# Performance work log

Hardware: AMD Instinct MI355X
Metric: run time of the kernel (lower is better)

Reference implementation:

```python
import jax, jax.numpy as jnp
import numpy as np

N_USERS = 100000
N_ITEMS = 50000
D = 64
NNZ = 4_800_000
N_HOPS = 3


def setup_inputs() -> dict:
    key = jax.random.key(0)
    k1, k2, k3, k4, k5 = jax.random.split(key, 5)
    n_nodes = N_USERS + N_ITEMS
    user_embed = jax.random.normal(k1, (N_USERS, D), dtype=jnp.float32) * 0.1
    item_embed = jax.random.normal(k2, (N_ITEMS, D), dtype=jnp.float32) * 0.1
    # COO indices of the symmetric-normalized interaction adjacency
    row = jax.random.randint(k3, (NNZ,), 0, n_nodes, dtype=jnp.int32)
    col = jax.random.randint(k4, (NNZ,), 0, n_nodes, dtype=jnp.int32)
    # normalized adjacency values ~ 1/deg scale
    vals = jax.random.uniform(k5, (NNZ,), dtype=jnp.float32) * (1.0 / 32.0)
    return {"user_embed": user_embed, "item_embed": item_embed,
            "row": row, "col": col, "vals": vals}


def reference(user_embed, item_embed, row, col, vals):
    """GraphConv.forward with perturbed=False (path used in M4.forward).

    torch.sparse.mm(A, X) over COO == segment_sum(vals * X[col], row).
    """
    n_users = user_embed.shape[0]
    n_nodes = n_users + item_embed.shape[0]
    ego = jnp.concatenate([user_embed, item_embed], axis=0)  # [N, D]

    def spmm(x):
        return jax.ops.segment_sum(vals[:, None] * x[col], row,
                                   num_segments=n_nodes)

    hop_outs = []
    for _ in range(N_HOPS):
        ego = spmm(ego)
        hop_outs.append(ego)
    layer_embeddings = hop_outs[0]  # k == 0 hop (layer_cl path)
    all_embeddings = jnp.mean(jnp.stack(hop_outs, axis=1), axis=1)  # [N, D]

    return (all_embeddings[:n_users], all_embeddings[n_users:],
            layer_embeddings[:n_users], layer_embeddings[n_users:])
```

## Files before the change

### kernel.cpp

```cpp
#include <hip/hip_runtime.h>
#include <hip/hip_bf16.h>


#define D 64
typedef unsigned short u16;

#define NBP   512
#define BSH   9
#define TILE  2048
#define FCAP  4608

__device__ __forceinline__ float bf2f(u16 h) {
    union { unsigned int u; float f; } c;
    c.u = ((unsigned int)h) << 16;
    return c.f;
}
__device__ __forceinline__ u16 f2bf(float f) {
    union { float f; unsigned int u; } c; c.f = f;
    unsigned int r = c.u + 0x7FFFu + ((c.u >> 16) & 1u);
    return (u16)(r >> 16);
}

struct U4 { u16 a, b, c, d; } __attribute__((aligned(8)));

__global__ void detect_kernel(const u16* __restrict__ emb,
                              const u16* __restrict__ vals,
                              int* __restrict__ flags) {
    int lane = threadIdx.x;
    int se = 0, sv = 0;
    for (int k = 0; k < 16; ++k) {
        int idx = (lane * 16 + k) * 2;
        u16 he = emb[idx];
        int ee = (he >> 7) & 0xFF;
        if (ee >= 100 && ee < 127) se++;
        u16 hv = vals[idx];
        int ev = (hv >> 7) & 0xFF;
        if ((hv >> 15) == 0 && ev >= 60 && ev < 123) sv++;
    }
    atomicAdd(&flags[0], se);
    atomicAdd(&flags[1], sv);
}

__global__ __launch_bounds__(256)
void convert_kernel(const void* __restrict__ ue, const void* __restrict__ ie,
                    const int* __restrict__ flags, u16* __restrict__ x0,
                    int total, int usz) {
    int i = (blockIdx.x * blockDim.x + threadIdx.x) * 4;
    if (i >= total) return;
    const void* src = (i < usz) ? ue : ie;
    int off = (i < usz) ? i : i - usz;
    U4 o;
    if (flags[0] >= 512) {
        o = *(const U4*)((const u16*)src + off);
    } else {
        const float4 v = *(const float4*)((const float*)src + off);
        o.a = f2bf(v.x); o.b = f2bf(v.y); o.c = f2bf(v.z); o.d = f2bf(v.w);
    }
    *(U4*)(x0 + i) = o;
}

__global__ __launch_bounds__(256)
void bhist_kernel(const int* __restrict__ row, int* __restrict__ bcnt, int nnz) {
    __shared__ int h[NBP];
    int t = threadIdx.x;
    h[t] = 0; h[t + 256] = 0;
    __syncthreads();
    for (int i = blockIdx.x * 256 + t; i < nnz; i += gridDim.x * 256)
        atomicAdd(&h[row[i] >> BSH], 1);
    __syncthreads();
    if (h[t])       atomicAdd(&bcnt[t],       h[t]);
    if (h[t + 256]) atomicAdd(&bcnt[t + 256], h[t + 256]);
}

__global__ void bscan_kernel(const int* __restrict__ bcnt, int* __restrict__ bbase,
                             int* __restrict__ bcursor, int nb, int nnz) {
    __shared__ int buf[NBP];
    int t = threadIdx.x;
    int v = (t < nb) ? bcnt[t] : 0;
    buf[t] = v;
    __syncthreads();
    for (int off = 1; off < NBP; off <<= 1) {
        int y = (t >= off) ? buf[t - off] : 0;
        __syncthreads();
        buf[t] += y;
        __syncthreads();
    }
    int excl = buf[t] - v;
    bbase[t] = excl;
    bcursor[t] = excl;
    if (t == 0) bbase[nb] = nnz;
}

__global__ __launch_bounds__(256)
void coarse_kernel(const int* __restrict__ row, const int* __restrict__ col,
                   const void* __restrict__ vals, const int* __restrict__ flags,
                   int* __restrict__ bcursor, int2* __restrict__ es2, int nnz) {
    __shared__ int2 ebuf[TILE];
    __shared__ u16  slotb[TILE];
    __shared__ int  hcnt[NBP], hscn[NBP], goff[NBP];
    int t = threadIdx.x;
    int base = blockIdx.x * TILE;
    int tcnt = nnz - base; if (tcnt > TILE) tcnt = TILE;
    bool vbf = (flags[1] >= 512);

    hcnt[t] = 0; hcnt[t + 256] = 0;
    __syncthreads();

    int eb[8], er[8], ep[8], ev[8];
#pragma unroll
    for (int k = 0; k < 8; ++k) {
        int i = base + k * 256 + t;
        eb[k] = -1;
        if (k * 256 + t < tcnt) {
            int r = row[i];
            int c = col[i];
            float v = vbf ? bf2f(((const u16*)vals)[i]) : ((const float*)vals)[i];
            eb[k] = r >> BSH;
            ep[k] = ((r & 511) << 18) | c;
            ev[k] = __float_as_int(v);
            er[k] = atomicAdd(&hcnt[eb[k]], 1);
        }
    }
    __syncthreads();
    hscn[t] = hcnt[t]; hscn[t + 256] = hcnt[t + 256];
    __syncthreads();
    for (int off = 1; off < NBP; off <<= 1) {
        int a0 = (t >= off) ? hscn[t - off] : 0;
        int a1 = (t + 256 >= off) ? hscn[t + 256 - off] : 0;
        __syncthreads();
        hscn[t] += a0; hscn[t + 256] += a1;
        __syncthreads();
    }
#pragma unroll
    for (int k = 0; k < 8; ++k) {
        if (eb[k] >= 0) {
            int slot = hscn[eb[k]] - hcnt[eb[k]] + er[k];
            ebuf[slot] = make_int2(ep[k], ev[k]);
            slotb[slot] = (u16)eb[k];
        }
    }
    __syncthreads();
    if (hcnt[t] > 0)       goff[t]       = atomicAdd(&bcursor[t],       hcnt[t]);
    if (hcnt[t + 256] > 0) goff[t + 256] = atomicAdd(&bcursor[t + 256], hcnt[t + 256]);
    __syncthreads();
#pragma unroll
    for (int k = 0; k < 8; ++k) {
        int p = k * 256 + t;
        if (p < tcnt) {
            int b = slotb[p];
            int dest = goff[b] + (p - (hscn[b] - hcnt[b]));
            es2[dest] = ebuf[p];
        }
    }
}

__global__ __launch_bounds__(512)
void fine_kernel(const int2* __restrict__ es2, const int* __restrict__ bbase,
                 int2* __restrict__ es, int* __restrict__ rp, int n, int nnz) {
    __shared__ int2 obuf[FCAP];
    __shared__ int hist[512], scn[512], cur[128];
    int b = blockIdx.x, t = threadIdx.x;
    int r0 = b << BSH;
    int s = bbase[b], e = bbase[b + 1];
    if (b == 0 && t == 0) rp[n] = nnz;

    hist[t] = 0;
    __syncthreads();
    for (int i = s + t; i < e; i += 512)
        atomicAdd(&hist[(unsigned)es2[i].x >> 18], 1);
    __syncthreads();
    scn[t] = hist[t];
    __syncthreads();
    for (int off = 1; off < 512; off <<= 1) {
        int a = (t >= off) ? scn[t - off] : 0;
        __syncthreads();
        scn[t] += a;
        __syncthreads();
    }
    {
        int ex = scn[t] - hist[t];
        int r = r0 + t;
        if (r < n) rp[r] = s + ex;
    }

    for (int c = 0; c < 4; ++c) {
        int qb = c * 128;
        int q0 = qb ? scn[qb - 1] : 0;
        int qcnt = scn[qb + 127] - q0;
        int ds = s + q0;
        bool fit = (qcnt <= FCAP);
        if (t < 128) {
            int ex = scn[qb + t] - hist[qb + t];
            cur[t] = fit ? (ex - q0) : (s + ex);
        }
        __syncthreads();
        if (fit) {
            for (int i = s + t; i < e; i += 512) {
                int2 p = es2[i];
                int rl = (unsigned)p.x >> 18;
                if ((rl >> 7) == c) {
                    int pos = atomicAdd(&cur[rl & 127], 1);
                    obuf[pos] = make_int2(p.x & 0x3FFFF, p.y);
                }
            }
            __syncthreads();
            for (int p2 = t; p2 < qcnt; p2 += 512)
                es[ds + p2] = obuf[p2];
            __syncthreads();
        } else {
            for (int i = s + t; i < e; i += 512) {
                int2 p = es2[i];
                int rl = (unsigned)p.x >> 18;
                if ((rl >> 7) == c) {
                    int pos = atomicAdd(&cur[rl & 127], 1);
                    es[pos] = make_int2(p.x & 0x3FFFF, p.y);
                }
            }
            __syncthreads();
        }
    }
}


__global__ __launch_bounds__(256)
void spmm_kernel(const u16* __restrict__ x, u16* __restrict__ y,
                 const int* __restrict__ rp, const int2* __restrict__ es, int n) {
    int wid  = (blockIdx.x * blockDim.x + threadIdx.x) >> 6;
    int lane = threadIdx.x & 63;
    int qt   = lane >> 4;
    int sub  = lane & 15;
    int r    = (wid << 2) + qt;
    int e = 0, e1 = 0;
    if (r < n) { e = rp[r]; e1 = rp[r + 1]; }
    const u16* xs = x + (sub << 2);

    float a0 = 0.f, a1 = 0.f, a2 = 0.f, a3 = 0.f;
    float b0 = 0.f, b1 = 0.f, b2 = 0.f, b3 = 0.f;

    for (; e + 8 <= e1; e += 8) {
        int2 p0 = es[e],     p1 = es[e + 1], p2 = es[e + 2], p3 = es[e + 3];
        int2 p4 = es[e + 4], p5 = es[e + 5], p6 = es[e + 6], p7 = es[e + 7];
        U4 v0 = *(const U4*)(xs + (p0.x << 6));
        U4 v1 = *(const U4*)(xs + (p1.x << 6));
        U4 v2 = *(const U4*)(xs + (p2.x << 6));
        U4 v3 = *(const U4*)(xs + (p3.x << 6));
        U4 v4 = *(const U4*)(xs + (p4.x << 6));
        U4 v5 = *(const U4*)(xs + (p5.x << 6));
        U4 v6 = *(const U4*)(xs + (p6.x << 6));
        U4 v7 = *(const U4*)(xs + (p7.x << 6));
        float w0 = __int_as_float(p0.y), w1 = __int_as_float(p1.y);
        float w2 = __int_as_float(p2.y), w3 = __int_as_float(p3.y);
        float w4 = __int_as_float(p4.y), w5 = __int_as_float(p5.y);
        float w6 = __int_as_float(p6.y), w7 = __int_as_float(p7.y);
        a0 += w0 * bf2f(v0.a); a1 += w0 * bf2f(v0.b); a2 += w0 * bf2f(v0.c); a3 += w0 * bf2f(v0.d);
        b0 += w1 * bf2f(v1.a); b1 += w1 * bf2f(v1.b); b2 += w1 * bf2f(v1.c); b3 += w1 * bf2f(v1.d);
        a0 += w2 * bf2f(v2.a); a1 += w2 * bf2f(v2.b); a2 += w2 * bf2f(v2.c); a3 += w2 * bf2f(v2.d);
        b0 += w3 * bf2f(v3.a); b1 += w3 * bf2f(v3.b); b2 += w3 * bf2f(v3.c); b3 += w3 * bf2f(v3.d);
        a0 += w4 * bf2f(v4.a); a1 += w4 * bf2f(v4.b); a2 += w4 * bf2f(v4.c); a3 += w4 * bf2f(v4.d);
        b0 += w5 * bf2f(v5.a); b1 += w5 * bf2f(v5.b); b2 += w5 * bf2f(v5.c); b3 += w5 * bf2f(v5.d);
        a0 += w6 * bf2f(v6.a); a1 += w6 * bf2f(v6.b); a2 += w6 * bf2f(v6.c); a3 += w6 * bf2f(v6.d);
        b0 += w7 * bf2f(v7.a); b1 += w7 * bf2f(v7.b); b2 += w7 * bf2f(v7.c); b3 += w7 * bf2f(v7.d);
    }
    for (; e < e1; ++e) {
        int2 p = es[e];
        U4 v = *(const U4*)(xs + (p.x << 6));
        float w = __int_as_float(p.y);
        a0 += w * bf2f(v.a); a1 += w * bf2f(v.b); a2 += w * bf2f(v.c); a3 += w * bf2f(v.d);
    }
    if (r < n) {
        U4 o;
        o.a = f2bf(a0 + b0); o.b = f2bf(a1 + b1);
        o.c = f2bf(a2 + b2); o.d = f2bf(a3 + b3);
        *(U4*)(y + (r << 6) + (sub << 2)) = o;
    }
}

__global__ __launch_bounds__(256)
void spmm_last_kernel(const u16* __restrict__ x2, const u16* __restrict__ x1,
                      float* __restrict__ out,
                      const int* __restrict__ rp, const int2* __restrict__ es, int n) {
    int wid  = (blockIdx.x * blockDim.x + threadIdx.x) >> 6;
    int lane = threadIdx.x & 63;
    int qt   = lane >> 4;
    int sub  = lane & 15;
    int r    = (wid << 2) + qt;
    int e = 0, e1 = 0;
    if (r < n) { e = rp[r]; e1 = rp[r + 1]; }
    const u16* xs = x2 + (sub << 2);

    float a0 = 0.f, a1 = 0.f, a2 = 0.f, a3 = 0.f;
    float b0 = 0.f, b1 = 0.f, b2 = 0.f, b3 = 0.f;

    for (; e + 8 <= e1; e += 8) {
        int2 p0 = es[e],     p1 = es[e + 1], p2 = es[e + 2], p3 = es[e + 3];
        int2 p4 = es[e + 4], p5 = es[e + 5], p6 = es[e + 6], p7 = es[e + 7];
        U4 v0 = *(const U4*)(xs + (p0.x << 6));
        U4 v1 = *(const U4*)(xs + (p1.x << 6));
        U4 v2 = *(const U4*)(xs + (p2.x << 6));
        U4 v3 = *(const U4*)(xs + (p3.x << 6));
        U4 v4 = *(const U4*)(xs + (p4.x << 6));
        U4 v5 = *(const U4*)(xs + (p5.x << 6));
        U4 v6 = *(const U4*)(xs + (p6.x << 6));
        U4 v7 = *(const U4*)(xs + (p7.x << 6));
        float w0 = __int_as_float(p0.y), w1 = __int_as_float(p1.y);
        float w2 = __int_as_float(p2.y), w3 = __int_as_float(p3.y);
        float w4 = __int_as_float(p4.y), w5 = __int_as_float(p5.y);
        float w6 = __int_as_float(p6.y), w7 = __int_as_float(p7.y);
        a0 += w0 * bf2f(v0.a); a1 += w0 * bf2f(v0.b); a2 += w0 * bf2f(v0.c); a3 += w0 * bf2f(v0.d);
        b0 += w1 * bf2f(v1.a); b1 += w1 * bf2f(v1.b); b2 += w1 * bf2f(v1.c); b3 += w1 * bf2f(v1.d);
        a0 += w2 * bf2f(v2.a); a1 += w2 * bf2f(v2.b); a2 += w2 * bf2f(v2.c); a3 += w2 * bf2f(v2.d);
        b0 += w3 * bf2f(v3.a); b1 += w3 * bf2f(v3.b); b2 += w3 * bf2f(v3.c); b3 += w3 * bf2f(v3.d);
        a0 += w4 * bf2f(v4.a); a1 += w4 * bf2f(v4.b); a2 += w4 * bf2f(v4.c); a3 += w4 * bf2f(v4.d);
        b0 += w5 * bf2f(v5.a); b1 += w5 * bf2f(v5.b); b2 += w5 * bf2f(v5.c); b3 += w5 * bf2f(v5.d);
        a0 += w6 * bf2f(v6.a); a1 += w6 * bf2f(v6.b); a2 += w6 * bf2f(v6.c); a3 += w6 * bf2f(v6.d);
        b0 += w7 * bf2f(v7.a); b1 += w7 * bf2f(v7.b); b2 += w7 * bf2f(v7.c); b3 += w7 * bf2f(v7.d);
    }
    for (; e < e1; ++e) {
        int2 p = es[e];
        U4 v = *(const U4*)(xs + (p.x << 6));
        float w = __int_as_float(p.y);
        a0 += w * bf2f(v.a); a1 += w * bf2f(v.b); a2 += w * bf2f(v.c); a3 += w * bf2f(v.d);
    }
    if (r < n) {
        int idx = (r << 6) + (sub << 2);
        U4 h1v = *(const U4*)(x1 + idx);
        U4 h2v = *(const U4*)(x2 + idx);
        float h1a = bf2f(h1v.a), h1b = bf2f(h1v.b), h1c = bf2f(h1v.c), h1d = bf2f(h1v.d);
        float h2a = bf2f(h2v.a), h2b = bf2f(h2v.b), h2c = bf2f(h2v.c), h2d = bf2f(h2v.d);
        float4 o;
        o.x = (h1a + h2a + (a0 + b0)) * (1.0f / 3.0f);
        o.y = (h1b + h2b + (a1 + b1)) * (1.0f / 3.0f);
        o.z = (h1c + h2c + (a2 + b2)) * (1.0f / 3.0f);
        o.w = (h1d + h2d + (a3 + b3)) * (1.0f / 3.0f);
        *(float4*)(out + idx) = o;
        float4 l;
        l.x = h1a; l.y = h1b; l.z = h1c; l.w = h1d;
        *(float4*)(out + (size_t)n * D + idx) = l;
    }
}


extern "C" void kernel_launch(void* const* d_in, const int* in_sizes, int n_in,
                              void* d_out, int out_size, void* d_ws, size_t ws_size,
                              hipStream_t stream) {
    const void* ue   = d_in[0];
    const void* ie   = d_in[1];
    const int*  row  = (const int*)d_in[2];
    const int*  col  = (const int*)d_in[3];
    const void* vals = d_in[4];

    const int nu  = in_sizes[0] / D;
    const int ni  = in_sizes[1] / D;
    const int n   = nu + ni;
    const int nnz = in_sizes[2];

    char* ws = (char*)d_ws;
    u16*  X0     = (u16*)ws;   ws += (size_t)n * D * sizeof(u16);
    u16*  X1     = (u16*)ws;   ws += (size_t)n * D * sizeof(u16);
    u16*  X2     = (u16*)ws;   ws += (size_t)n * D * sizeof(u16);
    int2* es2    = (int2*)X1;
    int2* es     = (int2*)ws;  ws += (size_t)nnz * sizeof(int2);
    int*  rp     = (int*)ws;   ws += (size_t)(n + 1) * sizeof(int);
    int*  bcnt   = (int*)ws;   ws += NBP * sizeof(int);
    int*  flags  = (int*)ws;   ws += 2 * sizeof(int);
    int*  bbase  = (int*)ws;   ws += (NBP + 1) * sizeof(int);
    int*  bcursor= (int*)ws;   ws += NBP * sizeof(int);

    const int tb = 256;
    const int rblocks = (n + 15) / 16;
    const int cblocks = (n * D / 4 + tb - 1) / tb;
    const int NB      = (n + 511) / 512;
    const int coarseb = (nnz + TILE - 1) / TILE;

    hipMemsetAsync(bcnt, 0, (NBP + 2) * sizeof(int), stream);
    detect_kernel <<<1, 64, 0, stream>>>((const u16*)ue, (const u16*)vals, flags);
    convert_kernel<<<cblocks, tb, 0, stream>>>(ue, ie, flags, X0, n * D, nu * D);
    bhist_kernel  <<<512, tb, 0, stream>>>(row, bcnt, nnz);
    bscan_kernel  <<<1, NBP, 0, stream>>>(bcnt, bbase, bcursor, NB, nnz);
    coarse_kernel <<<coarseb, tb, 0, stream>>>(row, col, vals, flags, bcursor, es2, nnz);
    fine_kernel   <<<NB, 512, 0, stream>>>(es2, bbase, es, rp, n, nnz);

    spmm_kernel     <<<rblocks, tb, 0, stream>>>(X0, X1, rp, es, n);
    spmm_kernel     <<<rblocks, tb, 0, stream>>>(X1, X2, rp, es, n);
    spmm_last_kernel<<<rblocks, tb, 0, stream>>>(X2, X1, (float*)d_out, rp, es, n);
}
```

Before: 610.3 us.

## Sub-sort edges within each row by column bucket in fine_kernel

In the in-shared-memory path of fine_kernel, edges are now bucketed by (row, column>>13) through an extra histogram pass and a block-wide scan, so each row's edges come out roughly ordered by column range. The goal is better locality for the gathers of x[col] in the SpMM hops. The cost is an extra pass over es2 per chunk, two more 4096-entry shared arrays that may lower occupancy, and more block-wide synchronisation in the preprocessing kernel.

New measurement: 660.6 us. +8.2%, slower.

```diff
diff --git a/kernel.cpp b/kernel.cpp
--- a/kernel.cpp
+++ b/kernel.cpp
@@ -9,6 +9,8 @@
 #define BSH   9
 #define TILE  2048
 #define FCAP  4608
+#define CGS   32
+#define KH    (128 * CGS)
 
 __device__ __forceinline__ float bf2f(u16 h) {
     union { unsigned int u; float f; } c;
@@ -158,7 +160,8 @@
 void fine_kernel(const int2* __restrict__ es2, const int* __restrict__ bbase,
                  int2* __restrict__ es, int* __restrict__ rp, int n, int nnz) {
     __shared__ int2 obuf[FCAP];
-    __shared__ int hist[512], scn[512], cur[128];
+    __shared__ int hist[512], scn[512], wsum[512], cur[128];
+    __shared__ int kh[KH], cur2[KH];
     int b = blockIdx.x, t = threadIdx.x;
     int r0 = b << BSH;
     int s = bbase[b], e = bbase[b + 1];
@@ -189,18 +192,47 @@
         int qcnt = scn[qb + 127] - q0;
         int ds = s + q0;
         bool fit = (qcnt <= FCAP);
-        if (t < 128) {
-            int ex = scn[qb + t] - hist[qb + t];
-            cur[t] = fit ? (ex - q0) : (s + ex);
-        }
-        __syncthreads();
         if (fit) {
+#pragma unroll
+            for (int j = 0; j < KH / 512; ++j) kh[t + j * 512] = 0;
+            __syncthreads();
             for (int i = s + t; i < e; i += 512) {
                 int2 p = es2[i];
                 int rl = (unsigned)p.x >> 18;
                 if ((rl >> 7) == c) {
-                    int pos = atomicAdd(&cur[rl & 127], 1);
-                    obuf[pos] = make_int2(p.x & 0x3FFFF, p.y);
+                    int key = ((rl & 127) << 5) | ((p.x & 0x3FFFF) >> 13);
+                    atomicAdd(&kh[key], 1);
+                }
+            }
+            __syncthreads();
+            int cnt8[8], loc8[8], acc = 0;
+#pragma unroll
+            for (int k = 0; k < 8; ++k) {
+                cnt8[k] = kh[t * 8 + k];
+                acc += cnt8[k];
+                loc8[k] = acc;
+            }
+            wsum[t] = acc;
+            __syncthreads();
+            for (int off = 1; off < 512; off <<= 1) {
+                int a = (t >= off) ? wsum[t - off] : 0;
+                __syncthreads();
+                wsum[t] += a;
+                __syncthreads();
+            }
+            int kb = wsum[t] - acc;
+#pragma unroll
+            for (int k = 0; k < 8; ++k)
+                cur2[t * 8 + k] = kb + loc8[k] - cnt8[k];
+            __syncthreads();
+            for (int i = s + t; i < e; i += 512) {
+                int2 p = es2[i];
+                int rl = (unsigned)p.x >> 18;
+                if ((rl >> 7) == c) {
+                    int cl = p.x & 0x3FFFF;
+                    int key = ((rl & 127) << 5) | (cl >> 13);
+                    int pos = atomicAdd(&cur2[key], 1);
+                    obuf[pos] = make_int2(cl, p.y);
                 }
             }
             __syncthreads();
@@ -208,6 +240,11 @@
                 es[ds + p2] = obuf[p2];
             __syncthreads();
         } else {
+            if (t < 128) {
+                int ex = scn[qb + t] - hist[qb + t];
+                cur[t] = s + ex;
+            }
+            __syncthreads();
             for (int i = s + t; i < e; i += 512) {
                 int2 p = es2[i];
                 int rl = (unsigned)p.x >> 18;
```

## Split feature dimension into two halves to shrink gathered working set

Applied to the files above, without the earlier changes.

Embeddings are stored as two separate 32-wide halves, and all three SpMM hops run independently on each half, giving six launches instead of three. Each half table is half the size, so the random gathers hit a smaller working set that fits better in L2/MALL cache. The cost is reading the edge list and row pointers twice and doing narrower 4-byte gathers per lane, which means more gather instructions per byte moved.

Result: slower. 772.3 us (+26.5%).

```diff
diff --git a/kernel.cpp b/kernel.cpp
--- a/kernel.cpp
+++ b/kernel.cpp
@@ -22,6 +22,7 @@
 }
 
 struct U4 { u16 a, b, c, d; } __attribute__((aligned(8)));
+struct U2 { u16 a, b; } __attribute__((aligned(4)));
 
 __global__ void detect_kernel(const u16* __restrict__ emb,
                               const u16* __restrict__ vals,
@@ -43,7 +44,8 @@
 
 __global__ __launch_bounds__(256)
 void convert_kernel(const void* __restrict__ ue, const void* __restrict__ ie,
-                    const int* __restrict__ flags, u16* __restrict__ x0,
+                    const int* __restrict__ flags,
+                    u16* __restrict__ xa, u16* __restrict__ xb,
                     int total, int usz) {
     int i = (blockIdx.x * blockDim.x + threadIdx.x) * 4;
     if (i >= total) return;
@@ -56,7 +58,9 @@
         const float4 v = *(const float4*)((const float*)src + off);
         o.a = f2bf(v.x); o.b = f2bf(v.y); o.c = f2bf(v.z); o.d = f2bf(v.w);
     }
-    *(U4*)(x0 + i) = o;
+    int node = i >> 6, dim = i & 63;
+    u16* dst = (dim & 32) ? xb : xa;
+    *(U4*)(dst + (node << 5) + (dim & 31)) = o;
 }
 
 __global__ __launch_bounds__(256)
@@ -223,8 +227,8 @@
 
 
 __global__ __launch_bounds__(256)
-void spmm_kernel(const u16* __restrict__ x, u16* __restrict__ y,
-                 const int* __restrict__ rp, const int2* __restrict__ es, int n) {
+void spmmh_kernel(const u16* __restrict__ x, u16* __restrict__ y,
+                  const int* __restrict__ rp, const int2* __restrict__ es, int n) {
     int wid  = (blockIdx.x * blockDim.x + threadIdx.x) >> 6;
     int lane = threadIdx.x & 63;
     int qt   = lane >> 4;
@@ -232,53 +236,52 @@
     int r    = (wid << 2) + qt;
     int e = 0, e1 = 0;
     if (r < n) { e = rp[r]; e1 = rp[r + 1]; }
-    const u16* xs = x + (sub << 2);
-
-    float a0 = 0.f, a1 = 0.f, a2 = 0.f, a3 = 0.f;
-    float b0 = 0.f, b1 = 0.f, b2 = 0.f, b3 = 0.f;
+    const u16* xs = x + (sub << 1);
+
+    float a0 = 0.f, a1 = 0.f, b0 = 0.f, b1 = 0.f;
 
     for (; e + 8 <= e1; e += 8) {
         int2 p0 = es[e],     p1 = es[e + 1], p2 = es[e + 2], p3 = es[e + 3];
         int2 p4 = es[e + 4], p5 = es[e + 5], p6 = es[e + 6], p7 = es[e + 7];
-        U4 v0 = *(const U4*)(xs + (p0.x << 6));
-        U4 v1 = *(const U4*)(xs + (p1.x << 6));
-        U4 v2 = *(const U4*)(xs + (p2.x << 6));
-        U4 v3 = *(const U4*)(xs + (p3.x << 6));
-        U4 v4 = *(const U4*)(xs + (p4.x << 6));
-        U4 v5 = *(const U4*)(xs + (p5.x << 6));
-        U4 v6 = *(const U4*)(xs + (p6.x << 6));
-        U4 v7 = *(const U4*)(xs + (p7.x << 6));
+        U2 v0 = *(const U2*)(xs + (p0.x << 5));
+        U2 v1 = *(const U2*)(xs + (p1.x << 5));
+        U2 v2 = *(const U2*)(xs + (p2.x << 5));
+        U2 v3 = *(const U2*)(xs + (p3.x << 5));
+        U2 v4 = *(const U2*)(xs + (p4.x << 5));
+        U2 v5 = *(const U2*)(xs + (p5.x << 5));
+        U2 v6 = *(const U2*)(xs + (p6.x << 5));
+        U2 v7 = *(const U2*)(xs + (p7.x << 5));
         float w0 = __int_as_float(p0.y), w1 = __int_as_float(p1.y);
         float w2 = __int_as_float(p2.y), w3 = __int_as_float(p3.y);
         float w4 = __int_as_float(p4.y), w5 = __int_as_float(p5.y);
         float w6 = __int_as_float(p6.y), w7 = __int_as_float(p7.y);
-        a0 += w0 * bf2f(v0.a); a1 += w0 * bf2f(v0.b); a2 += w0 * bf2f(v0.c); a3 += w0 * bf2f(v0.d);
-        b0 += w1 * bf2f(v1.a); b1 += w1 * bf2f(v1.b); b2 += w1 * bf2f(v1.c); b3 += w1 * bf2f(v1.d);
-        a0 += w2 * bf2f(v2.a); a1 += w2 * bf2f(v2.b); a2 += w2 * bf2f(v2.c); a3 += w2 * bf2f(v2.d);
-        b0 += w3 * bf2f(v3.a); b1 += w3 * bf2f(v3.b); b2 += w3 * bf2f(v3.c); b3 += w3 * bf2f(v3.d);
-        a0 += w4 * bf2f(v4.a); a1 += w4 * bf2f(v4.b); a2 += w4 * bf2f(v4.c); a3 += w4 * bf2f(v4.d);
-        b0 += w5 * bf2f(v5.a); b1 += w5 * bf2f(v5.b); b2 += w5 * bf2f(v5.c); b3 += w5 * bf2f(v5.d);
-        a0 += w6 * bf2f(v6.a); a1 += w6 * bf2f(v6.b); a2 += w6 * bf2f(v6.c); a3 += w6 * bf2f(v6.d);
-        b0 += w7 * bf2f(v7.a); b1 += w7 * bf2f(v7.b); b2 += w7 * bf2f(v7.c); b3 += w7 * bf2f(v7.d);
+        a0 += w0 * bf2f(v0.a); a1 += w0 * bf2f(v0.b);
+        b0 += w1 * bf2f(v1.a); b1 += w1 * bf2f(v1.b);
+        a0 += w2 * bf2f(v2.a); a1 += w2 * bf2f(v2.b);
+        b0 += w3 * bf2f(v3.a); b1 += w3 * bf2f(v3.b);
+        a0 += w4 * bf2f(v4.a); a1 += w4 * bf2f(v4.b);
+        b0 += w5 * bf2f(v5.a); b1 += w5 * bf2f(v5.b);
+        a0 += w6 * bf2f(v6.a); a1 += w6 * bf2f(v6.b);
+        b0 += w7 * bf2f(v7.a); b1 += w7 * bf2f(v7.b);
     }
     for (; e < e1; ++e) {
         int2 p = es[e];
-        U4 v = *(const U4*)(xs + (p.x << 6));
+        U2 v = *(const U2*)(xs + (p.x << 5));
         float w = __int_as_float(p.y);
-        a0 += w * bf2f(v.a); a1 += w * bf2f(v.b); a2 += w * bf2f(v.c); a3 += w * bf2f(v.d);
+        a0 += w * bf2f(v.a); a1 += w * bf2f(v.b);
     }
     if (r < n) {
-        U4 o;
+        U2 o;
         o.a = f2bf(a0 + b0); o.b = f2bf(a1 + b1);
-        o.c = f2bf(a2 + b2); o.d = f2bf(a3 + b3);
-        *(U4*)(y + (r << 6) + (sub << 2)) = o;
-    }
-}
-
-__global__ __launch_bounds__(256)
-void spmm_last_kernel(const u16* __restrict__ x2, const u16* __restrict__ x1,
-                      float* __restrict__ out,
-                      const int* __restrict__ rp, const int2* __restrict__ es, int n) {
+        *(U2*)(y + (r << 5) + (sub << 1)) = o;
+    }
+}
+
+__global__ __launch_bounds__(256)
+void spmmh_last_kernel(const u16* __restrict__ x2, const u16* __restrict__ x1,
+                       float* __restrict__ out,
+                       const int* __restrict__ rp, const int2* __restrict__ es,
+                       int n, int hoff) {
     int wid  = (blockIdx.x * blockDim.x + threadIdx.x) >> 6;
     int lane = threadIdx.x & 63;
     int qt   = lane >> 4;
@@ -286,56 +289,53 @@
     int r    = (wid << 2) + qt;
     int e = 0, e1 = 0;
     if (r < n) { e = rp[r]; e1 = rp[r + 1]; }
-    const u16* xs = x2 + (sub << 2);
-
-    float a0 = 0.f, a1 = 0.f, a2 = 0.f, a3 = 0.f;
-    float b0 = 0.f, b1 = 0.f, b2 = 0.f, b3 = 0.f;
+    const u16* xs = x2 + (sub << 1);
+
+    float a0 = 0.f, a1 = 0.f, b0 = 0.f, b1 = 0.f;
 
     for (; e + 8 <= e1; e += 8) {
         int2 p0 = es[e],     p1 = es[e + 1], p2 = es[e + 2], p3 = es[e + 3];
         int2 p4 = es[e + 4], p5 = es[e + 5], p6 = es[e + 6], p7 = es[e + 7];
-        U4 v0 = *(const U4*)(xs + (p0.x << 6));
-        U4 v1 = *(const U4*)(xs + (p1.x << 6));
-        U4 v2 = *(const U4*)(xs + (p2.x << 6));
-        U4 v3 = *(const U4*)(xs + (p3.x << 6));
-        U4 v4 = *(const U4*)(xs + (p4.x << 6));
-        U4 v5 = *(const U4*)(xs + (p5.x << 6));
-        U4 v6 = *(const U4*)(xs + (p6.x << 6));
-        U4 v7 = *(const U4*)(xs + (p7.x << 6));
+        U2 v0 = *(const U2*)(xs + (p0.x << 5));
+        U2 v1 = *(const U2*)(xs + (p1.x << 5));
+        U2 v2 = *(const U2*)(xs + (p2.x << 5));
+        U2 v3 = *(const U2*)(xs + (p3.x << 5));
+        U2 v4 = *(const U2*)(xs + (p4.x << 5));
+        U2 v5 = *(const U2*)(xs + (p5.x << 5));
+        U2 v6 = *(const U2*)(xs + (p6.x << 5));
+        U2 v7 = *(const U2*)(xs + (p7.x << 5));
         float w0 = __int_as_float(p0.y), w1 = __int_as_float(p1.y);
         float w2 = __int_as_float(p2.y), w3 = __int_as_float(p3.y);
         float w4 = __int_as_float(p4.y), w5 = __int_as_float(p5.y);
         float w6 = __int_as_float(p6.y), w7 = __int_as_float(p7.y);
-        a0 += w0 * bf2f(v0.a); a1 += w0 * bf2f(v0.b); a2 += w0 * bf2f(v0.c); a3 += w0 * bf2f(v0.d);
-        b0 += w1 * bf2f(v1.a); b1 += w1 * bf2f(v1.b); b2 += w1 * bf2f(v1.c); b3 += w1 * bf2f(v1.d);
-        a0 += w2 * bf2f(v2.a); a1 += w2 * bf2f(v2.b); a2 += w2 * bf2f(v2.c); a3 += w2 * bf2f(v2.d);
-        b0 += w3 * bf2f(v3.a); b1 += w3 * bf2f(v3.b); b2 += w3 * bf2f(v3.c); b3 += w3 * bf2f(v3.d);
-        a0 += w4 * bf2f(v4.a); a1 += w4 * bf2f(v4.b); a2 += w4 * bf2f(v4.c); a3 += w4 * bf2f(v4.d);
-        b0 += w5 * bf2f(v5.a); b1 += w5 * bf2f(v5.b); b2 += w5 * bf2f(v5.c); b3 += w5 * bf2f(v5.d);
-        a0 += w6 * bf2f(v6.a); a1 += w6 * bf2f(v6.b); a2 += w6 * bf2f(v6.c); a3 += w6 * bf2f(v6.d);
-        b0 += w7 * bf2f(v7.a); b1 += w7 * bf2f(v7.b); b2 += w7 * bf2f(v7.c); b3 += w7 * bf2f(v7.d);
+        a0 += w0 * bf2f(v0.a); a1 += w0 * bf2f(v0.b);
+        b0 += w1 * bf2f(v1.a); b1 += w1 * bf2f(v1.b);
+        a0 += w2 * bf2f(v2.a); a1 += w2 * bf2f(v2.b);
+        b0 += w3 * bf2f(v3.a); b1 += w3 * bf2f(v3.b);
+        a0 += w4 * bf2f(v4.a); a1 += w4 * bf2f(v4.b);
+        b0 += w5 * bf2f(v5.a); b1 += w5 * bf2f(v5.b);
+        a0 += w6 * bf2f(v6.a); a1 += w6 * bf2f(v6.b);
+        b0 += w7 * bf2f(v7.a); b1 += w7 * bf2f(v7.b);
     }
     for (; e < e1; ++e) {
         int2 p = es[e];
-        U4 v = *(const U4*)(xs + (p.x << 6));
+        U2 v = *(const U2*)(xs + (p.x << 5));
         float w = __int_as_float(p.y);
-        a0 += w * bf2f(v.a); a1 += w * bf2f(v.b); a2 += w * bf2f(v.c); a3 += w * bf2f(v.d);
+        a0 += w * bf2f(v.a); a1 += w * bf2f(v.b);
     }
     if (r < n) {
-        int idx = (r << 6) + (sub << 2);
-        U4 h1v = *(const U4*)(x1 + idx);
-        U4 h2v = *(const U4*)(x2 + idx);
-        float h1a = bf2f(h1v.a), h1b = bf2f(h1v.b), h1c = bf2f(h1v.c), h1d = bf2f(h1v.d);
-        float h2a = bf2f(h2v.a), h2b = bf2f(h2v.b), h2c = bf2f(h2v.c), h2d = bf2f(h2v.d);
-        float4 o;
-        o.x = (h1a + h2a + (a0 + b0)) * (1.0f / 3.0f);
-        o.y = (h1b + h2b + (a1 + b1)) * (1.0f / 3.0f);
-        o.z = (h1c + h2c + (a2 + b2)) * (1.0f / 3.0f);
-        o.w = (h1d + h2d + (a3 + b3)) * (1.0f / 3.0f);
-        *(float4*)(out + idx) = o;
-        float4 l;
-        l.x = h1a; l.y = h1b; l.z = h1c; l.w = h1d;
-        *(float4*)(out + (size_t)n * D + idx) = l;
+        int hidx = (r << 5) + (sub << 1);
+        U2 h1v = *(const U2*)(x1 + hidx);
+        U2 h2v = *(const U2*)(x2 + hidx);
+        float h1a = bf2f(h1v.a), h1b = bf2f(h1v.b);
+        int oidx = (r << 6) + hoff + (sub << 1);
+        float2 o;
+        o.x = (h1a + bf2f(h2v.a) + (a0 + b0)) * (1.0f / 3.0f);
+        o.y = (h1b + bf2f(h2v.b) + (a1 + b1)) * (1.0f / 3.0f);
+        *(float2*)(out + oidx) = o;
+        float2 l;
+        l.x = h1a; l.y = h1b;
+        *(float2*)(out + (size_t)n * D + oidx) = l;
     }
 }
 
@@ -354,11 +354,15 @@
     const int n   = nu + ni;
     const int nnz = in_sizes[2];
 
+    const size_t hsz = (size_t)n * 32 * sizeof(u16);
     char* ws = (char*)d_ws;
-    u16*  X0     = (u16*)ws;   ws += (size_t)n * D * sizeof(u16);
-    u16*  X1     = (u16*)ws;   ws += (size_t)n * D * sizeof(u16);
-    u16*  X2     = (u16*)ws;   ws += (size_t)n * D * sizeof(u16);
-    int2* es2    = (int2*)X1;
+    u16*  X0a    = (u16*)ws;   ws += hsz;
+    u16*  X0b    = (u16*)ws;   ws += hsz;
+    u16*  X1a    = (u16*)ws;   ws += hsz;
+    u16*  X2a    = (u16*)ws;   ws += hsz;
+    u16*  X1b    = (u16*)ws;   ws += hsz;
+    u16*  X2b    = (u16*)ws;   ws += hsz;
+    int2* es2    = (int2*)X1a;
     int2* es     = (int2*)ws;  ws += (size_t)nnz * sizeof(int2);
     int*  rp     = (int*)ws;   ws += (size_t)(n + 1) * sizeof(int);
     int*  bcnt   = (int*)ws;   ws += NBP * sizeof(int);
@@ -374,13 +378,16 @@
 
     hipMemsetAsync(bcnt, 0, (NBP + 2) * sizeof(int), stream);
     detect_kernel <<<1, 64, 0, stream>>>((const u16*)ue, (const u16*)vals, flags);
-    convert_kernel<<<cblocks, tb, 0, stream>>>(ue, ie, flags, X0, n * D, nu * D);
+    convert_kernel<<<cblocks, tb, 0, stream>>>(ue, ie, flags, X0a, X0b, n * D, nu * D);
     bhist_kernel  <<<512, tb, 0, stream>>>(row, bcnt, nnz);
     bscan_kernel  <<<1, NBP, 0, stream>>>(bcnt, bbase, bcursor, NB, nnz);
     coarse_kernel <<<coarseb, tb, 0, stream>>>(row, col, vals, flags, bcursor, es2, nnz);
     fine_kernel   <<<NB, 512, 0, stream>>>(es2, bbase, es, rp, n, nnz);
 
-    spmm_kernel     <<<rblocks, tb, 0, stream>>>(X0, X1, rp, es, n);
-    spmm_kernel     <<<rblocks, tb, 0, stream>>>(X1, X2, rp, es, n);
-    spmm_last_kernel<<<rblocks, tb, 0, stream>>>(X2, X1, (float*)d_out, rp, es, n);
-}
+    spmmh_kernel     <<<rblocks, tb, 0, stream>>>(X0a, X1a, rp, es, n);
+    spmmh_kernel     <<<rblocks, tb, 0, stream>>>(X1a, X2a, rp, es, n);
+    spmmh_last_kernel<<<rblocks, tb, 0, stream>>>(X2a, X1a, (float*)d_out, rp, es, n, 0);
+    spmmh_kernel     <<<rblocks, tb, 0, stream>>>(X0b, X1b, rp, es, n);
+    spmmh_kernel     <<<rblocks, tb, 0, stream>>>(X1b, X2b, rp, es, n);
+    spmmh_last_kernel<<<rblocks, tb, 0, stream>>>(X2b, X1b, (float*)d_out, rp, es, n, 32);
+}
```
